# Optimization experiments

Measured on AMD Instinct MI355X. Metric: run time of the kernel, lower is better.

## Reference

```python
import jax, jax.numpy as jnp
import numpy as np

B, S, D = 128, 1024, 256
K = 512  # num_clusters


def setup_inputs() -> dict:
    key = jax.random.key(0)
    k1, = jax.random.split(key, 1)
    inputs = jax.random.normal(k1, (B, S, D), dtype=jnp.float32)
    # init centroids as the first K data points so no cluster is empty
    centroids = inputs.reshape(-1, D)[:K]
    return {"inputs": inputs, "centroids": centroids}


def reference(inputs, centroids):
    d = inputs.shape[-1]
    k = centroids.shape[0]
    x = inputs.reshape(-1, d)                      # [N, D]
    # squared euclidean distances via GEMM decomposition (avoids N x K x D tensor)
    x2 = jnp.sum(x * x, axis=1, keepdims=True)     # [N, 1]
    c2 = jnp.sum(centroids * centroids, axis=1)    # [K]
    dist = x2 - 2.0 * (x @ centroids.T) + c2       # [N, K]
    idx = jnp.argmin(dist, axis=-1)                # [N]
    clusters = jax.nn.one_hot(idx, k, dtype=x.dtype)   # [N, K]
    counts = jnp.sum(clusters, axis=0)             # [K]
    sums = jnp.einsum('nk,nd->kd', clusters, x)    # [K, D] scatter-reduce as GEMM
    new_centroids = sums / counts[:, None]         # [K, D]
    updated_centroids = 0.9 * centroids + 0.1 * new_centroids  # EMA update
    clusters_out = clusters.reshape(inputs.shape[:-1] + (k,))  # [B, S, K]
    return clusters_out, updated_centroids
```

## Files before the change

kernel.cpp:

```cpp
#include <hip/hip_runtime.h>
#include <hip/hip_fp16.h>

#define NPTS 131072
#define DIM  256
#define KTOT 512
#define GAP_T 0.2f

typedef unsigned short u16;
typedef _Float16 half8 __attribute__((ext_vector_type(8)));
typedef float floatx4 __attribute__((ext_vector_type(4)));

#define WS_MAIN_NEED 8394816u

__global__ __launch_bounds__(64)
void c2_kernel(const float* __restrict__ c, double* __restrict__ c2) {
  int k = blockIdx.x;
  int lane = threadIdx.x;
  const float* row = c + (size_t)k * DIM;
  double s = 0.0;
#pragma unroll
  for (int r = 0; r < DIM / 64; ++r) {
    float v = row[r * 64 + lane];
    s += (double)v * (double)v;
  }
#pragma unroll
  for (int off = 32; off > 0; off >>= 1) s += __shfl_down(s, off);
  if (lane == 0) c2[k] = s;
}

__global__ __launch_bounds__(64)
void prep_c_kernel(const float* __restrict__ c, double* __restrict__ c2,
                   u16* __restrict__ Ch, float* __restrict__ cT) {
  int k = blockIdx.x, lane = threadIdx.x;
  const float* row = c + (size_t)k * DIM;
  float4 v = ((const float4*)row)[lane];
  double s = (double)v.x * v.x + (double)v.y * v.y + (double)v.z * v.z + (double)v.w * v.w;
#pragma unroll
  for (int off = 32; off > 0; off >>= 1) s += __shfl_down(s, off);
  if (lane == 0) c2[k] = s;
  cT[(size_t)(lane * 4 + 0) * KTOT + k] = v.x;
  cT[(size_t)(lane * 4 + 1) * KTOT + k] = v.y;
  cT[(size_t)(lane * 4 + 2) * KTOT + k] = v.z;
  cT[(size_t)(lane * 4 + 3) * KTOT + k] = v.w;
  int cg = lane >> 1, h = lane & 1;
  int kc = cg >> 3, cc = cg & 7;
  union { _Float16 hh[4]; ushort4 u; } cvt;
  cvt.hh[0] = (_Float16)v.x; cvt.hh[1] = (_Float16)v.y;
  cvt.hh[2] = (_Float16)v.z; cvt.hh[3] = (_Float16)v.w;
  *(ushort4*)(Ch + (size_t)k * DIM + kc * 64 + (size_t)(cc ^ (k & 7)) * 8 + h * 4) = cvt.u;
}

__global__ __launch_bounds__(256)
void convert_x_kernel(const float* __restrict__ x, u16* __restrict__ Xh) {
  int id = blockIdx.x * 256 + threadIdx.x;
  int n = id >> 5;
  int cg = id & 31;
  int kc = cg >> 3, cc = cg & 7;
  const float4* src = (const float4*)(x + (size_t)n * DIM + cg * 8);
  float4 f0 = src[0], f1 = src[1];
  half8 hv;
  hv[0] = (_Float16)f0.x; hv[1] = (_Float16)f0.y; hv[2] = (_Float16)f0.z; hv[3] = (_Float16)f0.w;
  hv[4] = (_Float16)f1.x; hv[5] = (_Float16)f1.y; hv[6] = (_Float16)f1.z; hv[7] = (_Float16)f1.w;
  *(half8*)(Xh + (size_t)n * DIM + kc * 64 + (size_t)(cc ^ (n & 7)) * 8) = hv;
}

__device__ __forceinline__ void load_lds16(const void* g, void* l) {
  __builtin_amdgcn_global_load_lds((const __attribute__((address_space(1))) void*)g,
                                   (__attribute__((address_space(3))) void*)l, 16, 0, 0);
}

__global__ __launch_bounds__(256)
void gemm_topk_kernel(const u16* __restrict__ Xh, const u16* __restrict__ Ch,
                      const double* __restrict__ c2,
                      float* __restrict__ pv1, int* __restrict__ pk1, float* __restrict__ pv2) {
  __shared__ __align__(16) u16 Ah[128 * 64];
  __shared__ __align__(16) u16 Bh[128 * 64];
  __shared__ float mv1[128][2], mv2[128][2];
  __shared__ int mk1[128][2];

  const int tid = threadIdx.x;
  const int bx = blockIdx.x;
  const int nblk = (bx >> 3) & 3;
  const int mblk = (bx & 7) + ((bx >> 5) << 3);
  const int m0 = mblk * 128, n0 = nblk * 128;
  const int w = tid >> 6, lane = tid & 63;
  const int wm = (w & 1) * 64, wn = (w >> 1) * 64;
  const int lm = lane & 15, quad = lane >> 4;

  floatx4 acc[4][4] = {};

  for (int kc = 0; kc < 4; ++kc) {
    const int k0 = kc * 64;
    __syncthreads();
#pragma unroll
    for (int i = 0; i < 4; ++i) {
      int s = i * 256 + tid;
      int row = s >> 3, pos = s & 7;
      load_lds16(Xh + (size_t)(m0 + row) * DIM + k0 + pos * 8, Ah + (size_t)s * 8);
      load_lds16(Ch + (size_t)(n0 + row) * DIM + k0 + pos * 8, Bh + (size_t)s * 8);
    }
    __syncthreads();

#pragma unroll
    for (int s = 0; s < 2; ++s) {
      half8 ah[4], bh[4];
#pragma unroll
      for (int t = 0; t < 4; ++t) {
        int m = wm + t * 16 + lm;
        int pa = ((s * 4 + quad) ^ (m & 7)) * 8;
        ah[t] = *(const half8*)(Ah + (size_t)m * 64 + pa);
        int n = wn + t * 16 + lm;
        int pb = ((s * 4 + quad) ^ (n & 7)) * 8;
        bh[t] = *(const half8*)(Bh + (size_t)n * 64 + pb);
      }
#pragma unroll
      for (int mt = 0; mt < 4; ++mt)
#pragma unroll
        for (int nt = 0; nt < 4; ++nt)
          acc[mt][nt] = __builtin_amdgcn_mfma_f32_16x16x32_f16(ah[mt], bh[nt], acc[mt][nt], 0, 0, 0);
    }
  }

  float c2f[4];
#pragma unroll
  for (int nt = 0; nt < 4; ++nt) c2f[nt] = (float)c2[n0 + wn + nt * 16 + lm];

#pragma unroll
  for (int mt = 0; mt < 4; ++mt)
#pragma unroll
    for (int r = 0; r < 4; ++r) {
      float bv = 1e30f, sv = 1e30f;
      int bk = 0;
#pragma unroll
      for (int nt = 0; nt < 4; ++nt) {
        float v = c2f[nt] - 2.0f * acc[mt][nt][r];
        int n = n0 + wn + nt * 16 + lm;
        if (v < bv) { sv = bv; bv = v; bk = n; }
        else if (v < sv) sv = v;
      }
#pragma unroll
      for (int off = 1; off < 16; off <<= 1) {
        float ov = __shfl_xor(bv, off);
        int ok = __shfl_xor(bk, off);
        float osv = __shfl_xor(sv, off);
        if (ov < bv || (ov == bv && ok < bk)) { sv = fminf(bv, osv); bv = ov; bk = ok; }
        else sv = fminf(sv, ov);
      }
      if (lm == 0) {
        int mr = wm + mt * 16 + quad * 4 + r;
        int sl = w >> 1;
        mv1[mr][sl] = bv; mk1[mr][sl] = bk; mv2[mr][sl] = sv;
      }
    }
  __syncthreads();
  if (tid < 128) {
    float bv = mv1[tid][0], sv = mv2[tid][0];
    int bk = mk1[tid][0];
    float ov = mv1[tid][1], osv = mv2[tid][1];
    if (ov < bv) { sv = fminf(bv, osv); bv = ov; bk = mk1[tid][1]; }
    else sv = fminf(sv, ov);
    int m = m0 + tid;
    pv1[(size_t)nblk * NPTS + m] = bv;
    pk1[(size_t)nblk * NPTS + m] = bk;
    pv2[(size_t)nblk * NPTS + m] = sv;
  }
}

__global__ __launch_bounds__(256)
void combine_kernel(const float* __restrict__ pv1, const int* __restrict__ pk1,
                    const float* __restrict__ pv2, int* __restrict__ idx,
                    int* __restrict__ flagcnt, int* __restrict__ flaglist,
                    int* __restrict__ counts) {
  __shared__ int h[KTOT];
  int t = threadIdx.x;
#pragma unroll
  for (int i = 0; i < KTOT / 256; ++i) h[i * 256 + t] = 0;
  __syncthreads();
  int m = blockIdx.x * 256 + t;
  float bv = 1e30f, sv = 1e30f;
  int bk = 0;
#pragma unroll
  for (int b = 0; b < 4; ++b) {
    float v1 = pv1[(size_t)b * NPTS + m];
    int k1 = pk1[(size_t)b * NPTS + m];
    float v2 = pv2[(size_t)b * NPTS + m];
    if (v1 < bv) { sv = fminf(bv, v2); bv = v1; bk = k1; }
    else { sv = fminf(sv, v1); }
  }
  idx[m] = bk;
  atomicAdd(&h[bk], 1);
  if (sv - bv < GAP_T) {
    int p = atomicAdd(flagcnt, 1);
    flaglist[p] = m;
  }
  __syncthreads();
#pragma unroll
  for (int i = 0; i < KTOT / 256; ++i) {
    int v = h[i * 256 + t];
    if (v) atomicAdd(&counts[i * 256 + t], v);
  }
}

__global__ __launch_bounds__(256)
void refine_kernel(const float* __restrict__ x, const float* __restrict__ cT,
                   const double* __restrict__ c2, const int* __restrict__ flagcnt,
                   const int* __restrict__ flaglist, int* __restrict__ idx,
                   int* __restrict__ counts) {
  __shared__ __align__(16) float xs[DIM];
  __shared__ double rv[256];
  __shared__ int rk[256];
  int cnt = *(volatile const int*)flagcnt;
  const int ka = threadIdx.x, kb = threadIdx.x + 256;
  for (int i = blockIdx.x; i < cnt; i += gridDim.x) {
    __syncthreads();
    int m = flaglist[i];
    if (threadIdx.x < 64)
      ((float4*)xs)[threadIdx.x] = ((const float4*)(x + (size_t)m * DIM))[threadIdx.x];
    __syncthreads();
    double da = 0.0, db = 0.0;
#pragma unroll
    for (int dc = 0; dc < 8; ++dc) {
      float fa = 0.0f, fb = 0.0f;
#pragma unroll
      for (int d4 = 0; d4 < 8; ++d4) {
        float4 xv = ((const float4*)xs)[dc * 8 + d4];
        const float* ct0 = cT + (size_t)(dc * 32 + d4 * 4) * KTOT;
        fa = fmaf(xv.x, ct0[ka], fa);            fb = fmaf(xv.x, ct0[kb], fb);
        fa = fmaf(xv.y, ct0[KTOT + ka], fa);     fb = fmaf(xv.y, ct0[KTOT + kb], fb);
        fa = fmaf(xv.z, ct0[2 * KTOT + ka], fa); fb = fmaf(xv.z, ct0[2 * KTOT + kb], fb);
        fa = fmaf(xv.w, ct0[3 * KTOT + ka], fa); fb = fmaf(xv.w, ct0[3 * KTOT + kb], fb);
      }
      da += (double)fa; db += (double)fb;
    }
    double sa = c2[ka] - 2.0 * da, sb = c2[kb] - 2.0 * db;
    double bestv; int bestk;
    if (sa <= sb) { bestv = sa; bestk = ka; }
    else          { bestv = sb; bestk = kb; }
    rv[threadIdx.x] = bestv; rk[threadIdx.x] = bestk;
    __syncthreads();
    for (int off = 128; off > 0; off >>= 1) {
      if (threadIdx.x < off) {
        double v = rv[threadIdx.x + off]; int kk = rk[threadIdx.x + off];
        if (v < rv[threadIdx.x] || (v == rv[threadIdx.x] && kk < rk[threadIdx.x])) {
          rv[threadIdx.x] = v; rk[threadIdx.x] = kk;
        }
      }
      __syncthreads();
    }
    if (threadIdx.x == 0) {
      int bk = rk[0];
      int old = idx[m];
      if (bk != old) {
        idx[m] = bk;
        atomicSub(&counts[old], 1);
        atomicAdd(&counts[bk], 1);
      }
    }
  }
}

__global__ __launch_bounds__(256)
void onehot_kernel(const int* __restrict__ idx, float* __restrict__ out) {
  __shared__ int bk[32];
  int b = blockIdx.x;
  if (threadIdx.x < 32) bk[threadIdx.x] = idx[b * 32 + threadIdx.x];
  __syncthreads();
  float4* o = (float4*)(out + (size_t)b * 32 * KTOT);
#pragma unroll
  for (int j = 0; j < 16; ++j) {
    int f4 = j * 256 + threadIdx.x;
    int p = f4 >> 7;
    int n4 = (f4 & 127) * 4;
    int k = bk[p];
    float4 v;
    v.x = (k == n4 + 0) ? 1.0f : 0.0f;
    v.y = (k == n4 + 1) ? 1.0f : 0.0f;
    v.z = (k == n4 + 2) ? 1.0f : 0.0f;
    v.w = (k == n4 + 3) ? 1.0f : 0.0f;
    o[f4] = v;
  }
}

__global__ __launch_bounds__(512)
void scan_kernel(const int* __restrict__ counts, int* __restrict__ offsets,
                 int* __restrict__ cursors) {
  __shared__ int s[KTOT];
  int t = threadIdx.x;
  int mine = counts[t];
  s[t] = mine;
  __syncthreads();
  for (int off = 1; off < KTOT; off <<= 1) {
    int v = (t >= off) ? s[t - off] : 0;
    __syncthreads();
    s[t] += v;
    __syncthreads();
  }
  int excl = s[t] - mine;
  offsets[t] = excl;
  cursors[t] = excl;
  if (t == KTOT - 1) offsets[KTOT] = s[t];
}

__global__ __launch_bounds__(256)
void scatter_kernel(const int* __restrict__ idx, int* __restrict__ cursors,
                    int* __restrict__ plist) {
  int base = blockIdx.x * 1024 + threadIdx.x;
#pragma unroll
  for (int j = 0; j < 4; ++j) {
    int n = base + j * 256;
    int k = idx[n];
    int pos = atomicAdd(&cursors[k], 1);
    plist[pos] = n;
  }
}

__global__ __launch_bounds__(256)
void gathersum_flat_kernel(const float* __restrict__ x, const int* __restrict__ plist,
                           const int* __restrict__ offsets, float* __restrict__ sums) {
  __shared__ int offs[KTOT + 1];
  for (int t = threadIdx.x; t < KTOT + 1; t += 256) offs[t] = offsets[t];
  __syncthreads();
  const int w = threadIdx.x >> 6, lane = threadIdx.x & 63;
  const int wid = blockIdx.x * 4 + w;
  const int p0 = wid * 32, p1 = p0 + 32;

  int lo = 0, hi = KTOT;
  while (hi - lo > 1) { int mid = (lo + hi) >> 1; if (offs[mid] <= p0) lo = mid; else hi = mid; }
  int k = lo;

  float4 acc = make_float4(0.f, 0.f, 0.f, 0.f);
  bool any = false;
#pragma unroll 4
  for (int i = p0; i < p1; ++i) {
    while (i >= offs[k + 1]) {
      if (any) {
        float* dst = sums + (size_t)k * DIM + lane * 4;
        atomicAdd(dst + 0, acc.x); atomicAdd(dst + 1, acc.y);
        atomicAdd(dst + 2, acc.z); atomicAdd(dst + 3, acc.w);
        acc = make_float4(0.f, 0.f, 0.f, 0.f);
        any = false;
      }
      ++k;
    }
    int pid = plist[i];
    float4 v = ((const float4*)x)[(size_t)pid * 64 + lane];
    acc.x += v.x; acc.y += v.y; acc.z += v.z; acc.w += v.w;
    any = true;
  }
  if (any) {
    float* dst = sums + (size_t)k * DIM + lane * 4;
    atomicAdd(dst + 0, acc.x); atomicAdd(dst + 1, acc.y);
    atomicAdd(dst + 2, acc.z); atomicAdd(dst + 3, acc.w);
  }
}

__global__ __launch_bounds__(256)
void ema_kernel(const float* __restrict__ c, const float* __restrict__ sums,
                const int* __restrict__ counts, float* __restrict__ outc) {
  int k = blockIdx.x;
  int d = threadIdx.x;
  float cnt = (float)counts[k];
  size_t o = (size_t)k * DIM + d;
  float nc = sums[o] / cnt;
  outc[o] = 0.9f * c[o] + 0.1f * nc;
}

#define GB 4
#define SLICES 8
__global__ __launch_bounds__(256)
void sums_kernel(const float* __restrict__ x, const int* __restrict__ idx,
                 float* __restrict__ sums, int* __restrict__ counts) {
  const int groups = KTOT / GB;
  const int group = blockIdx.x % groups;
  const int slice = blockIdx.x / groups;
  const int kg0 = group * GB;
  const int tid = threadIdx.x;
  const int lane = tid & 63;
  const int w = tid >> 6;
  const int per_slice = NPTS / SLICES;
  const int nbeg = slice * per_slice;

  float4 acc[GB];
  int cnt[GB];
#pragma unroll
  for (int j = 0; j < GB; ++j) { acc[j] = make_float4(0.f, 0.f, 0.f, 0.f); cnt[j] = 0; }

  for (int it = 0; it < per_slice; it += 256) {
    int n = nbeg + it + tid;
    int k = idx[n];
#pragma unroll
    for (int j = 0; j < GB; ++j) {
      unsigned long long m = __ballot(k == kg0 + j);
      while (m) {
        int src = __ffsll((unsigned long long)m) - 1;
        int nn = __shfl(n, src);
        float4 v = ((const float4*)(x + (size_t)nn * DIM))[lane];
        acc[j].x += v.x; acc[j].y += v.y; acc[j].z += v.z; acc[j].w += v.w;
        cnt[j]++;
        m &= (m - 1);
      }
    }
  }

  __shared__ __align__(16) float lacc[4][GB][DIM];
  __shared__ int lcnt[4][GB];
#pragma unroll
  for (int j = 0; j < GB; ++j) ((float4*)&lacc[w][j][0])[lane] = acc[j];
  if (lane == 0) {
#pragma unroll
    for (int j = 0; j < GB; ++j) lcnt[w][j] = cnt[j];
  }
  __syncthreads();
#pragma unroll
  for (int j = 0; j < GB; ++j) {
    float s = lacc[0][j][tid] + lacc[1][j][tid] + lacc[2][j][tid] + lacc[3][j][tid];
    atomicAdd(&sums[(size_t)(kg0 + j) * DIM + tid], s);
  }
  if (tid < GB) {
    int ct = lcnt[0][tid] + lcnt[1][tid] + lcnt[2][tid] + lcnt[3][tid];
    atomicAdd(&counts[kg0 + tid], ct);
  }
}

#define MP 64
#define KT 64
#define DT 32
__global__ __launch_bounds__(256, 2)
void assign_kernel_r1(const float* __restrict__ x, const float* __restrict__ c,
                      const double* __restrict__ c2, float* __restrict__ out,
                      int* __restrict__ idx_out) {
  __shared__ __align__(16) float xs[DIM * MP];
  __shared__ __align__(16) float cs[DT * KT];
  const int tid = threadIdx.x;
  const int p0 = blockIdx.x * MP;
  const int tp = tid & 15;
  const int tk = tid >> 4;
  {
    const int p = tid >> 2;
    const int dg = tid & 3;
    const float4* x4 = (const float4*)(x + (size_t)(p0 + p) * DIM);
#pragma unroll
    for (int r = 0; r < 16; ++r) {
      int d4 = r * 4 + dg;
      float4 v = x4[d4];
      int dbase = d4 * 4;
      xs[(dbase + 0) * MP + p] = v.x;
      xs[(dbase + 1) * MP + p] = v.y;
      xs[(dbase + 2) * MP + p] = v.z;
      xs[(dbase + 3) * MP + p] = v.w;
    }
  }
  double best[4]; int bestk[4];
#pragma unroll
  for (int i = 0; i < 4; ++i) { best[i] = 1e300; bestk[i] = 0; }
  for (int kc = 0; kc < KTOT / KT; ++kc) {
    const int k0 = kc * KT;
    double dacc[4][4];
#pragma unroll
    for (int i = 0; i < 4; ++i)
#pragma unroll
      for (int j = 0; j < 4; ++j) dacc[i][j] = 0.0;
    for (int dc = 0; dc < DIM / DT; ++dc) {
      __syncthreads();
      {
        const int kl = tid >> 2;
        const int dg = tid & 3;
        const float4* c4 = (const float4*)(c + (size_t)(k0 + kl) * DIM + dc * DT);
#pragma unroll
        for (int h = 0; h < 2; ++h) {
          int dq = h * 4 + dg;
          float4 v = c4[dq];
          int dbase = dq * 4;
          cs[(dbase + 0) * KT + kl] = v.x;
          cs[(dbase + 1) * KT + kl] = v.y;
          cs[(dbase + 2) * KT + kl] = v.z;
          cs[(dbase + 3) * KT + kl] = v.w;
        }
      }
      __syncthreads();
      float acc[4][4];
#pragma unroll
      for (int i = 0; i < 4; ++i)
#pragma unroll
        for (int j = 0; j < 4; ++j) acc[i][j] = 0.0f;
#pragma unroll
      for (int d = 0; d < DT; ++d) {
        float4 xv = ((const float4*)(xs + (size_t)(dc * DT + d) * MP))[tp];
        float4 cv = ((const float4*)(cs + (size_t)d * KT))[tk];
        float xa[4] = {xv.x, xv.y, xv.z, xv.w};
        float ca[4] = {cv.x, cv.y, cv.z, cv.w};
#pragma unroll
        for (int i = 0; i < 4; ++i)
#pragma unroll
          for (int j = 0; j < 4; ++j) acc[i][j] = fmaf(xa[i], ca[j], acc[i][j]);
      }
#pragma unroll
      for (int i = 0; i < 4; ++i)
#pragma unroll
        for (int j = 0; j < 4; ++j) dacc[i][j] += (double)acc[i][j];
    }
#pragma unroll
    for (int j = 0; j < 4; ++j) {
      int k = k0 + tk * 4 + j;
      double c2v = c2[k];
#pragma unroll
      for (int i = 0; i < 4; ++i) {
        double s = c2v - 2.0 * dacc[i][j];
        if (s < best[i]) { best[i] = s; bestk[i] = k; }
      }
    }
  }
  __syncthreads();
  double* redv = (double*)cs;
  int* redk = (int*)xs;
  int* bk = (int*)xs + 1024;
#pragma unroll
  for (int i = 0; i < 4; ++i) {
    int p = tp * 4 + i;
    redv[tk * MP + p] = best[i];
    redk[tk * MP + p] = bestk[i];
  }
  __syncthreads();
  if (tid < MP) {
    int p = tid;
    double bv = redv[p]; int bkk = redk[p];
#pragma unroll
    for (int t = 1; t < 16; ++t) {
      double v = redv[t * MP + p]; int kk = redk[t * MP + p];
      if (v < bv || (v == bv && kk < bkk)) { bv = v; bkk = kk; }
    }
    bk[p] = bkk;
    idx_out[p0 + p] = bkk;
  }
  __syncthreads();
  float* orow = out + (size_t)p0 * KTOT;
  for (int l = tid; l < MP * KTOT; l += 256) {
    int p = l >> 9;
    int k = l & (KTOT - 1);
    orow[l] = (k == bk[p]) ? 1.0f : 0.0f;
  }
}

extern "C" void kernel_launch(void* const* d_in, const int* in_sizes, int n_in,
                              void* d_out, int out_size, void* d_ws, size_t ws_size,
                              hipStream_t stream) {
  const float* x = (const float*)d_in[0];
  const float* c = (const float*)d_in[1];
  float* out = (float*)d_out;
  float* outc = out + (size_t)NPTS * KTOT;

  char* ws = (char*)d_ws;

  if (ws_size >= WS_MAIN_NEED) {
    double* c2   = (double*)(ws + 0);
    u16* Ch      = (u16*)(ws + 4096);
    int* idx     = (int*)(ws + 528384);
    float* pv1   = (float*)(ws + 1052672);
    int* pk1     = (int*)(ws + 3149824);
    float* pv2   = (float*)(ws + 5246976);
    float* sums  = (float*)(ws + 7344128);
    int* counts  = (int*)(ws + 7868416);
    int* flagcnt = (int*)(ws + 7870464);
    int* flaglist= (int*)(ws + 7870528);
    int* offsets = (int*)(ws + 1052672);
    int* cursors = (int*)(ws + 1052672 + 4096);
    int* plist   = (int*)(ws + 5246976);
    u16* Xh      = (u16*)out;
    float* cT    = (float*)((char*)out + 134217728);

    hipMemsetAsync(sums, 0, (size_t)(KTOT * DIM + KTOT) * 4, stream);
    hipMemsetAsync(flagcnt, 0, 64, stream);
    prep_c_kernel<<<KTOT, 64, 0, stream>>>(c, c2, Ch, cT);
    convert_x_kernel<<<NPTS * 32 / 256, 256, 0, stream>>>(x, Xh);
    gemm_topk_kernel<<<4096, 256, 0, stream>>>(Xh, Ch, c2, pv1, pk1, pv2);
    combine_kernel<<<NPTS / 256, 256, 0, stream>>>(pv1, pk1, pv2, idx, flagcnt, flaglist, counts);
    refine_kernel<<<1024, 256, 0, stream>>>(x, cT, c2, flagcnt, flaglist, idx, counts);
    onehot_kernel<<<NPTS / 32, 256, 0, stream>>>(idx, out);
    scan_kernel<<<1, 512, 0, stream>>>(counts, offsets, cursors);
    scatter_kernel<<<NPTS / 1024, 256, 0, stream>>>(idx, cursors, plist);
    gathersum_flat_kernel<<<NPTS / 32 / 4, 256, 0, stream>>>(x, plist, offsets, sums);
    ema_kernel<<<KTOT, DIM, 0, stream>>>(c, sums, counts, outc);
  } else {
    double* c2  = (double*)ws;
    int* idx    = (int*)(ws + 4096);
    float* sums = (float*)(ws + 4096 + 524288);
    int* counts = (int*)(ws + 4096 + 524288 + 524288);
    hipMemsetAsync(sums, 0, (size_t)(KTOT * DIM + KTOT) * 4, stream);
    c2_kernel<<<KTOT, 64, 0, stream>>>(c, c2);
    assign_kernel_r1<<<NPTS / MP, 256, 0, stream>>>(x, c, c2, out, idx);
    sums_kernel<<<(KTOT / GB) * SLICES, 256, 0, stream>>>(x, idx, sums, counts);
    ema_kernel<<<KTOT, DIM, 0, stream>>>(c, sums, counts, outc);
  }
}
```

Measured before the change: 805.6 us.

## Load GEMM fragments directly from global memory, dropping LDS staging

The GEMM kernel no longer stages X and C tiles through shared memory with global_load_lds and barriers. Each wave now reads its half8 MFMA fragments straight from global memory through per-row pointers. The XOR swizzle in the fp16 conversion kernels is removed to match the plain row-major layout. This removes LDS traffic and __syncthreads, but each wave re-reads data that the others in the block also fetch, so the kernel leans on L1/L2 hits and loses the coalesced block-wide loads.

```diff
diff --git a/kernel.cpp b/kernel.cpp
--- a/kernel.cpp
+++ b/kernel.cpp
@@ -42,39 +42,29 @@
   cT[(size_t)(lane * 4 + 1) * KTOT + k] = v.y;
   cT[(size_t)(lane * 4 + 2) * KTOT + k] = v.z;
   cT[(size_t)(lane * 4 + 3) * KTOT + k] = v.w;
-  int cg = lane >> 1, h = lane & 1;
-  int kc = cg >> 3, cc = cg & 7;
   union { _Float16 hh[4]; ushort4 u; } cvt;
   cvt.hh[0] = (_Float16)v.x; cvt.hh[1] = (_Float16)v.y;
   cvt.hh[2] = (_Float16)v.z; cvt.hh[3] = (_Float16)v.w;
-  *(ushort4*)(Ch + (size_t)k * DIM + kc * 64 + (size_t)(cc ^ (k & 7)) * 8 + h * 4) = cvt.u;
+  *(ushort4*)(Ch + (size_t)k * DIM + lane * 4) = cvt.u;
 }
 
 __global__ __launch_bounds__(256)
 void convert_x_kernel(const float* __restrict__ x, u16* __restrict__ Xh) {
   int id = blockIdx.x * 256 + threadIdx.x;
   int n = id >> 5;
-  int cg = id & 31;
-  int kc = cg >> 3, cc = cg & 7;
-  const float4* src = (const float4*)(x + (size_t)n * DIM + cg * 8);
+  int j = id & 31;
+  const float4* src = (const float4*)(x + (size_t)n * DIM + j * 8);
   float4 f0 = src[0], f1 = src[1];
   half8 hv;
   hv[0] = (_Float16)f0.x; hv[1] = (_Float16)f0.y; hv[2] = (_Float16)f0.z; hv[3] = (_Float16)f0.w;
   hv[4] = (_Float16)f1.x; hv[5] = (_Float16)f1.y; hv[6] = (_Float16)f1.z; hv[7] = (_Float16)f1.w;
-  *(half8*)(Xh + (size_t)n * DIM + kc * 64 + (size_t)(cc ^ (n & 7)) * 8) = hv;
-}
-
-__device__ __forceinline__ void load_lds16(const void* g, void* l) {
-  __builtin_amdgcn_global_load_lds((const __attribute__((address_space(1))) void*)g,
-                                   (__attribute__((address_space(3))) void*)l, 16, 0, 0);
+  *(half8*)(Xh + (size_t)n * DIM + j * 8) = hv;
 }
 
 __global__ __launch_bounds__(256)
 void gemm_topk_kernel(const u16* __restrict__ Xh, const u16* __restrict__ Ch,
                       const double* __restrict__ c2,
                       float* __restrict__ pv1, int* __restrict__ pk1, float* __restrict__ pv2) {
-  __shared__ __align__(16) u16 Ah[128 * 64];
-  __shared__ __align__(16) u16 Bh[128 * 64];
   __shared__ float mv1[128][2], mv2[128][2];
   __shared__ int mk1[128][2];
 
@@ -87,31 +77,26 @@
   const int wm = (w & 1) * 64, wn = (w >> 1) * 64;
   const int lm = lane & 15, quad = lane >> 4;
 
+  const u16* pA[4];
+  const u16* pB[4];
+#pragma unroll
+  for (int t = 0; t < 4; ++t) {
+    pA[t] = Xh + (size_t)(m0 + wm + t * 16 + lm) * DIM + quad * 8;
+    pB[t] = Ch + (size_t)(n0 + wn + t * 16 + lm) * DIM + quad * 8;
+  }
+
   floatx4 acc[4][4] = {};
 
+#pragma unroll
   for (int kc = 0; kc < 4; ++kc) {
-    const int k0 = kc * 64;
-    __syncthreads();
-#pragma unroll
-    for (int i = 0; i < 4; ++i) {
-      int s = i * 256 + tid;
-      int row = s >> 3, pos = s & 7;
-      load_lds16(Xh + (size_t)(m0 + row) * DIM + k0 + pos * 8, Ah + (size_t)s * 8);
-      load_lds16(Ch + (size_t)(n0 + row) * DIM + k0 + pos * 8, Bh + (size_t)s * 8);
-    }
-    __syncthreads();
-
 #pragma unroll
     for (int s = 0; s < 2; ++s) {
+      const int ko = kc * 64 + s * 32;
       half8 ah[4], bh[4];
 #pragma unroll
       for (int t = 0; t < 4; ++t) {
-        int m = wm + t * 16 + lm;
-        int pa = ((s * 4 + quad) ^ (m & 7)) * 8;
-        ah[t] = *(const half8*)(Ah + (size_t)m * 64 + pa);
-        int n = wn + t * 16 + lm;
-        int pb = ((s * 4 + quad) ^ (n & 7)) * 8;
-        bh[t] = *(const half8*)(Bh + (size_t)n * 64 + pb);
+        ah[t] = *(const half8*)(pA[t] + ko);
+        bh[t] = *(const half8*)(pB[t] + ko);
       }
 #pragma unroll
       for (int mt = 0; mt < 4; ++mt)
```

After: 845.3 us. +4.9%, slower.

## Fuse x fp16 conversion into GEMM and split refinement into pair and full paths

Applied to the files above, without the earlier changes.

Drops the separate convert_x pass: the GEMM kernel now reads fp32 x directly, converts to fp16 and writes it swizzled into LDS. The top-k epilogue now tracks the second-best index and counts candidates within a wider margin. Combine uses these to send points to either a cheap two-centroid exact check or the full 512-centroid refinement, which shrinks the costly full refine work. The tradeoff is more GEMM epilogue work, synchronous register loads instead of async LDS loads for x, and flag lists capped at 32768 entries per path, which could drop refinements if that many points are flagged.

```diff
diff --git a/kernel.cpp b/kernel.cpp
--- a/kernel.cpp
+++ b/kernel.cpp
@@ -4,13 +4,21 @@
 #define NPTS 131072
 #define DIM  256
 #define KTOT 512
-#define GAP_T 0.2f
+#define GAP_PAIR 0.2f
+#define GAP_FULL 0.4f
 
 typedef unsigned short u16;
 typedef _Float16 half8 __attribute__((ext_vector_type(8)));
 typedef float floatx4 __attribute__((ext_vector_type(4)));
 
+union F16U { _Float16 f; unsigned short u; };
+
 #define WS_MAIN_NEED 8394816u
+
+__device__ __forceinline__ void ins2(float v, int k, float& B, int& KB, float& S, int& KS) {
+  if (v < B || (v == B && k < KB)) { S = B; KS = KB; B = v; KB = k; }
+  else if (v < S || (v == S && k < KS)) { S = v; KS = k; }
+}
 
 __global__ __launch_bounds__(64)
 void c2_kernel(const float* __restrict__ c, double* __restrict__ c2) {
@@ -50,33 +58,19 @@
   *(ushort4*)(Ch + (size_t)k * DIM + kc * 64 + (size_t)(cc ^ (k & 7)) * 8 + h * 4) = cvt.u;
 }
 
-__global__ __launch_bounds__(256)
-void convert_x_kernel(const float* __restrict__ x, u16* __restrict__ Xh) {
-  int id = blockIdx.x * 256 + threadIdx.x;
-  int n = id >> 5;
-  int cg = id & 31;
-  int kc = cg >> 3, cc = cg & 7;
-  const float4* src = (const float4*)(x + (size_t)n * DIM + cg * 8);
-  float4 f0 = src[0], f1 = src[1];
-  half8 hv;
-  hv[0] = (_Float16)f0.x; hv[1] = (_Float16)f0.y; hv[2] = (_Float16)f0.z; hv[3] = (_Float16)f0.w;
-  hv[4] = (_Float16)f1.x; hv[5] = (_Float16)f1.y; hv[6] = (_Float16)f1.z; hv[7] = (_Float16)f1.w;
-  *(half8*)(Xh + (size_t)n * DIM + kc * 64 + (size_t)(cc ^ (n & 7)) * 8) = hv;
-}
-
 __device__ __forceinline__ void load_lds16(const void* g, void* l) {
   __builtin_amdgcn_global_load_lds((const __attribute__((address_space(1))) void*)g,
                                    (__attribute__((address_space(3))) void*)l, 16, 0, 0);
 }
 
 __global__ __launch_bounds__(256)
-void gemm_topk_kernel(const u16* __restrict__ Xh, const u16* __restrict__ Ch,
+void gemm_topk_kernel(const float* __restrict__ x, const u16* __restrict__ Ch,
                       const double* __restrict__ c2,
-                      float* __restrict__ pv1, int* __restrict__ pk1, float* __restrict__ pv2) {
+                      float* __restrict__ pv1, int* __restrict__ pkk, unsigned* __restrict__ pgg) {
   __shared__ __align__(16) u16 Ah[128 * 64];
   __shared__ __align__(16) u16 Bh[128 * 64];
-  __shared__ float mv1[128][2], mv2[128][2];
-  __shared__ int mk1[128][2];
+  __shared__ float mb[128][2], msv[128][2], mbf[128];
+  __shared__ int mkb[128][2], mks[128][2], scnt[128][2];
 
   const int tid = threadIdx.x;
   const int bx = blockIdx.x;
@@ -96,8 +90,21 @@
     for (int i = 0; i < 4; ++i) {
       int s = i * 256 + tid;
       int row = s >> 3, pos = s & 7;
-      load_lds16(Xh + (size_t)(m0 + row) * DIM + k0 + pos * 8, Ah + (size_t)s * 8);
-      load_lds16(Ch + (size_t)(n0 + row) * DIM + k0 + pos * 8, Bh + (size_t)s * 8);
+      size_t go = (size_t)(n0 + row) * DIM + k0 + pos * 8;
+      load_lds16(Ch + go, Bh + (size_t)s * 8);
+    }
+#pragma unroll
+    for (int i = 0; i < 4; ++i) {
+      int s = i * 256 + tid;
+      int row = s >> 3, kg = s & 7;
+      const float4* gx = (const float4*)(x + (size_t)(m0 + row) * DIM + k0 + kg * 8);
+      float4 f0 = gx[0], f1 = gx[1];
+      float fv[8] = {f0.x, f0.y, f0.z, f0.w, f1.x, f1.y, f1.z, f1.w};
+      half8 hv;
+#pragma unroll
+      for (int e = 0; e < 8; ++e) hv[e] = (_Float16)fv[e];
+      int pos = kg ^ (row & 7);
+      *(half8*)(Ah + (size_t)row * 64 + pos * 8) = hv;
     }
     __syncthreads();
 
@@ -125,50 +132,76 @@
 #pragma unroll
   for (int nt = 0; nt < 4; ++nt) c2f[nt] = (float)c2[n0 + wn + nt * 16 + lm];
 
+  __syncthreads();
 #pragma unroll
   for (int mt = 0; mt < 4; ++mt)
 #pragma unroll
     for (int r = 0; r < 4; ++r) {
       float bv = 1e30f, sv = 1e30f;
-      int bk = 0;
+      int bk = 0x7fffffff, sk = 0x7fffffff;
 #pragma unroll
       for (int nt = 0; nt < 4; ++nt) {
         float v = c2f[nt] - 2.0f * acc[mt][nt][r];
         int n = n0 + wn + nt * 16 + lm;
-        if (v < bv) { sv = bv; bv = v; bk = n; }
-        else if (v < sv) sv = v;
+        if (v < bv || (v == bv && n < bk)) { sv = bv; sk = bk; bv = v; bk = n; }
+        else if (v < sv || (v == sv && n < sk)) { sv = v; sk = n; }
       }
 #pragma unroll
       for (int off = 1; off < 16; off <<= 1) {
-        float ov = __shfl_xor(bv, off);
-        int ok = __shfl_xor(bk, off);
-        float osv = __shfl_xor(sv, off);
-        if (ov < bv || (ov == bv && ok < bk)) { sv = fminf(bv, osv); bv = ov; bk = ok; }
-        else sv = fminf(sv, ov);
+        float ov = __shfl_xor(bv, off), osv = __shfl_xor(sv, off);
+        int ok = __shfl_xor(bk, off), osk = __shfl_xor(sk, off);
+        if (ov < bv || (ov == bv && ok < bk)) {
+          if (bv < osv || (bv == osv && bk < osk)) { sv = bv; sk = bk; }
+          else { sv = osv; sk = osk; }
+          bv = ov; bk = ok;
+        } else if (ov < sv || (ov == sv && ok < sk)) { sv = ov; sk = ok; }
       }
       if (lm == 0) {
         int mr = wm + mt * 16 + quad * 4 + r;
         int sl = w >> 1;
-        mv1[mr][sl] = bv; mk1[mr][sl] = bk; mv2[mr][sl] = sv;
+        mb[mr][sl] = bv; mkb[mr][sl] = bk; msv[mr][sl] = sv; mks[mr][sl] = sk;
       }
     }
   __syncthreads();
   if (tid < 128) {
-    float bv = mv1[tid][0], sv = mv2[tid][0];
-    int bk = mk1[tid][0];
-    float ov = mv1[tid][1], osv = mv2[tid][1];
-    if (ov < bv) { sv = fminf(bv, osv); bv = ov; bk = mk1[tid][1]; }
-    else sv = fminf(sv, ov);
+    float B = mb[tid][0], S = msv[tid][0];
+    int KB = mkb[tid][0], KS = mks[tid][0];
+    ins2(mb[tid][1], mkb[tid][1], B, KB, S, KS);
+    ins2(msv[tid][1], mks[tid][1], B, KB, S, KS);
+    mb[tid][0] = B; mkb[tid][0] = KB; msv[tid][0] = S; mks[tid][0] = KS;
+    mbf[tid] = B;
+  }
+  __syncthreads();
+#pragma unroll
+  for (int mt = 0; mt < 4; ++mt)
+#pragma unroll
+    for (int r = 0; r < 4; ++r) {
+      int mr = wm + mt * 16 + quad * 4 + r;
+      float thr = mbf[mr] + GAP_FULL;
+      int cnt = 0;
+#pragma unroll
+      for (int nt = 0; nt < 4; ++nt)
+        cnt += (c2f[nt] - 2.0f * acc[mt][nt][r] < thr) ? 1 : 0;
+#pragma unroll
+      for (int off = 1; off < 16; off <<= 1) cnt += __shfl_xor(cnt, off);
+      if (lm == 0) scnt[mr][w >> 1] = cnt;
+    }
+  __syncthreads();
+  if (tid < 128) {
+    float B = mb[tid][0], S = msv[tid][0];
+    int KB = mkb[tid][0], KS = mks[tid][0];
+    int C = scnt[tid][0] + scnt[tid][1];
     int m = m0 + tid;
-    pv1[(size_t)nblk * NPTS + m] = bv;
-    pk1[(size_t)nblk * NPTS + m] = bk;
-    pv2[(size_t)nblk * NPTS + m] = sv;
-  }
-}
-
-__global__ __launch_bounds__(256)
-void combine_kernel(const float* __restrict__ pv1, const int* __restrict__ pk1,
-                    const float* __restrict__ pv2, int* __restrict__ idx,
+    F16U cv; cv.f = (_Float16)(S - B);
+    pv1[(size_t)nblk * NPTS + m] = B;
+    pkk[(size_t)nblk * NPTS + m] = KB | (KS << 16);
+    pgg[(size_t)nblk * NPTS + m] = (unsigned)cv.u | ((unsigned)C << 16);
+  }
+}
+
+__global__ __launch_bounds__(256)
+void combine_kernel(const float* __restrict__ pv1, const int* __restrict__ pkk,
+                    const unsigned* __restrict__ pgg, int* __restrict__ idx,
                     int* __restrict__ flagcnt, int* __restrict__ flaglist,
                     int* __restrict__ counts) {
   __shared__ int h[KTOT];
@@ -177,21 +210,36 @@
   for (int i = 0; i < KTOT / 256; ++i) h[i * 256 + t] = 0;
   __syncthreads();
   int m = blockIdx.x * 256 + t;
-  float bv = 1e30f, sv = 1e30f;
-  int bk = 0;
+  float B = 1e30f, S = 1e30f;
+  int KB = 0x7fffffff, KS = 0x7fffffff;
+  float bb[4]; int cc[4];
 #pragma unroll
   for (int b = 0; b < 4; ++b) {
-    float v1 = pv1[(size_t)b * NPTS + m];
-    int k1 = pk1[(size_t)b * NPTS + m];
-    float v2 = pv2[(size_t)b * NPTS + m];
-    if (v1 < bv) { sv = fminf(bv, v2); bv = v1; bk = k1; }
-    else { sv = fminf(sv, v1); }
-  }
-  idx[m] = bk;
-  atomicAdd(&h[bk], 1);
-  if (sv - bv < GAP_T) {
-    int p = atomicAdd(flagcnt, 1);
-    flaglist[p] = m;
+    float bv = pv1[(size_t)b * NPTS + m];
+    int kk = pkk[(size_t)b * NPTS + m];
+    unsigned gg = pgg[(size_t)b * NPTS + m];
+    int kb_ = kk & 0xffff, ks_ = (kk >> 16) & 0xffff;
+    F16U cv; cv.u = (unsigned short)(gg & 0xffffu);
+    float sv = bv + (float)cv.f;
+    bb[b] = bv; cc[b] = (int)(gg >> 16);
+    ins2(bv, kb_, B, KB, S, KS);
+    ins2(sv, ks_, B, KB, S, KS);
+  }
+  idx[m] = KB;
+  atomicAdd(&h[KB], 1);
+  int tot = 0;
+#pragma unroll
+  for (int b = 0; b < 4; ++b)
+    if (bb[b] < B + GAP_FULL) tot += cc[b];
+  if (tot >= 3) {
+    int p = atomicAdd(&flagcnt[0], 1);
+    if (p < 32768) flaglist[p] = m;
+  } else if (tot == 2 && (S - B) < GAP_PAIR) {
+    int p = atomicAdd(&flagcnt[1], 1);
+    if (p < 32768) {
+      flaglist[32768 + p] = m;
+      flaglist[65536 + p] = KB | (KS << 16);
+    }
   }
   __syncthreads();
 #pragma unroll
@@ -202,10 +250,44 @@
 }
 
 __global__ __launch_bounds__(256)
-void refine_kernel(const float* __restrict__ x, const float* __restrict__ cT,
-                   const double* __restrict__ c2, const int* __restrict__ flagcnt,
-                   const int* __restrict__ flaglist, int* __restrict__ idx,
-                   int* __restrict__ counts) {
+void pair_refine_kernel(const float* __restrict__ x, const float* __restrict__ c,
+                        const double* __restrict__ c2, const int* __restrict__ flagcnt,
+                        const int* __restrict__ flaglist, int* __restrict__ idx,
+                        int* __restrict__ counts) {
+  int cnt = *(volatile const int*)(flagcnt + 1);
+  const int w = threadIdx.x >> 6, lane = threadIdx.x & 63;
+  for (int e = blockIdx.x * 4 + w; e < cnt; e += gridDim.x * 4) {
+    int m = flaglist[32768 + e];
+    int kk = flaglist[65536 + e];
+    int ka = kk & 0xffff, kb = (kk >> 16) & 0xffff;
+    float4 xv = ((const float4*)(x + (size_t)m * DIM))[lane];
+    float4 av = ((const float4*)(c + (size_t)ka * DIM))[lane];
+    float4 bv = ((const float4*)(c + (size_t)kb * DIM))[lane];
+    float fa = fmaf(xv.x, av.x, fmaf(xv.y, av.y, fmaf(xv.z, av.z, xv.w * av.w)));
+    float fb = fmaf(xv.x, bv.x, fmaf(xv.y, bv.y, fmaf(xv.z, bv.z, xv.w * bv.w)));
+    double da = (double)fa, db = (double)fb;
+#pragma unroll
+    for (int off = 32; off > 0; off >>= 1) {
+      da += __shfl_down(da, off);
+      db += __shfl_down(db, off);
+    }
+    if (lane == 0) {
+      double sa = c2[ka] - 2.0 * da, sb = c2[kb] - 2.0 * db;
+      int wk = (sb < sa || (sb == sa && kb < ka)) ? kb : ka;
+      if (wk != ka) {
+        idx[m] = wk;
+        atomicSub(&counts[ka], 1);
+        atomicAdd(&counts[wk], 1);
+      }
+    }
+  }
+}
+
+__global__ __launch_bounds__(256)
+void full_refine_kernel(const float* __restrict__ x, const float* __restrict__ cT,
+                        const double* __restrict__ c2, const int* __restrict__ flagcnt,
+                        const int* __restrict__ flaglist, int* __restrict__ idx,
+                        int* __restrict__ counts) {
   __shared__ __align__(16) float xs[DIM];
   __shared__ double rv[256];
   __shared__ int rk[256];
@@ -556,8 +638,8 @@
     u16* Ch      = (u16*)(ws + 4096);
     int* idx     = (int*)(ws + 528384);
     float* pv1   = (float*)(ws + 1052672);
-    int* pk1     = (int*)(ws + 3149824);
-    float* pv2   = (float*)(ws + 5246976);
+    int* pkk     = (int*)(ws + 3149824);
+    unsigned* pgg= (unsigned*)(ws + 5246976);
     float* sums  = (float*)(ws + 7344128);
     int* counts  = (int*)(ws + 7868416);
     int* flagcnt = (int*)(ws + 7870464);
@@ -565,16 +647,15 @@
     int* offsets = (int*)(ws + 1052672);
     int* cursors = (int*)(ws + 1052672 + 4096);
     int* plist   = (int*)(ws + 5246976);
-    u16* Xh      = (u16*)out;
     float* cT    = (float*)((char*)out + 134217728);
 
     hipMemsetAsync(sums, 0, (size_t)(KTOT * DIM + KTOT) * 4, stream);
     hipMemsetAsync(flagcnt, 0, 64, stream);
     prep_c_kernel<<<KTOT, 64, 0, stream>>>(c, c2, Ch, cT);
-    convert_x_kernel<<<NPTS * 32 / 256, 256, 0, stream>>>(x, Xh);
-    gemm_topk_kernel<<<4096, 256, 0, stream>>>(Xh, Ch, c2, pv1, pk1, pv2);
-    combine_kernel<<<NPTS / 256, 256, 0, stream>>>(pv1, pk1, pv2, idx, flagcnt, flaglist, counts);
-    refine_kernel<<<1024, 256, 0, stream>>>(x, cT, c2, flagcnt, flaglist, idx, counts);
+    gemm_topk_kernel<<<4096, 256, 0, stream>>>(x, Ch, c2, pv1, pkk, pgg);
+    combine_kernel<<<NPTS / 256, 256, 0, stream>>>(pv1, pkk, pgg, idx, flagcnt, flaglist, counts);
+    full_refine_kernel<<<256, 256, 0, stream>>>(x, cT, c2, flagcnt, flaglist, idx, counts);
+    pair_refine_kernel<<<256, 256, 0, stream>>>(x, c, c2, flagcnt, flaglist, idx, counts);
     onehot_kernel<<<NPTS / 32, 256, 0, stream>>>(idx, out);
     scan_kernel<<<1, 512, 0, stream>>>(counts, offsets, cursors);
     scatter_kernel<<<NPTS / 1024, 256, 0, stream>>>(idx, cursors, plist);
```

After: 830.0 us. 3.0% more time.
